# Kernel tuning notes

Hardware: AMD Instinct MI355X
Metric: run time of the kernel (lower is better)

## Reference

```python
import jax, jax.numpy as jnp
import numpy as np

TOP_K = 2


def setup_inputs() -> dict:
    key = jax.random.key(0)
    k1, k2, k3, k4 = jax.random.split(key, 4)
    B, S, D, F, E = 4, 512, 512, 2048, 16
    hidden_states = jax.random.normal(k1, (B, S, D), dtype=jnp.float32)
    gate_weight = jax.random.normal(k2, (E, D), dtype=jnp.float32) * 0.02
    w1 = jax.random.normal(k3, (E, F, D), dtype=jnp.float32) * 0.02
    w2 = jax.random.normal(k4, (E, D, F), dtype=jnp.float32) * 0.02
    return {"hidden_states": hidden_states, "gate_weight": gate_weight, "w1": w1, "w2": w2}


def reference(hidden_states, gate_weight, w1, w2):
    B, S, D = hidden_states.shape
    E = gate_weight.shape[0]
    x = hidden_states.reshape(-1, D)  # [T, D]

    # fused_top_k_routing: logits = x @ Wg^T, top-k, softmax over the k values
    gate_logits = x @ gate_weight.T  # [T, E]
    top_vals, top_idx = jax.lax.top_k(gate_logits, TOP_K)  # [T, k]
    routing_w = jax.nn.softmax(top_vals, axis=-1)  # [T, k]

    # _prepare_expert_inputs: token t goes to expert e iff e in its top-k
    mask = jnp.any(top_idx[:, :, None] == jnp.arange(E)[None, None, :], axis=1)  # [T, E] bool

    # Expert FFN on routed tokens, computed densely over (token, expert) pairs then masked.
    # h[t,e,f] = silu(x_t @ W1_e^T)
    h = jax.nn.silu(jnp.einsum('td,efd->tef', x, w1))  # [T, E, F]
    counts = jnp.sum(mask, axis=0)  # [E]
    h_sum = jnp.einsum('tef,te->ef', h, mask.astype(h.dtype))  # [E, F]
    h_mean = h_sum / jnp.maximum(counts, 1)[:, None].astype(h.dtype)

    # fused_expert_scatter_gather uses expert_outputs[e].mean(dim=0);
    # mean(W2 @ act) = W2 @ mean(act) since W2 is linear.
    y_mean = jnp.einsum('ef,edf->ed', h_mean, w2)  # [E, D]
    y_mean = jnp.where((counts > 0)[:, None], y_mean, 0.0)

    # per-token combine: sum_k w_k * mean_output[expert_k]
    out = jnp.einsum('tk,tkd->td', routing_w, y_mean[top_idx])  # [T, D]
    return out.reshape(B, S, D)
```

## Files before the change

kernel.cpp:

```cpp
#include <hip/hip_runtime.h>

#define NTOK   2048
#define DIM    512
#define FDIM   2048
#define NEXP   16
#define CAP    768
#define BT2    128
#define NTB    (CAP / BT2)

typedef __bf16 bf16x8 __attribute__((ext_vector_type(8)));
typedef float  floatx4 __attribute__((ext_vector_type(4)));

#define WS_COUNTS    0
#define WS_TOPIDX    4096
#define WS_ROUTW     20480
#define WS_HMEAN     36864
#define WS_YMEAN     167936
#define WS_XG        200704
#define WS_ZERO_BYTES 167936


__device__ __forceinline__ void async_lds16(const void* g, void* l) {
    __builtin_amdgcn_global_load_lds(
        (const __attribute__((address_space(1))) void*)g,
        (__attribute__((address_space(3))) void*)l, 16, 0, 0);
}

__global__ __launch_bounds__(256) void k1_route_gather(
    const float* __restrict__ x, const float* __restrict__ gw,
    int* __restrict__ counts, int* __restrict__ top_idx,
    float* __restrict__ routw, __bf16* __restrict__ Xg)
{
    __shared__ float xt[16 * DIM];
    __shared__ float lg[16][17];
    __shared__ int   gde[16][2];
    __shared__ int   gdp[16][2];
    const int tid = threadIdx.x;
    const int t0  = blockIdx.x * 16;

    {
        const float4* src = (const float4*)(x + (size_t)t0 * DIM);
        float4* dst = (float4*)xt;
        #pragma unroll
        for (int i = 0; i < 8; ++i) dst[i * 256 + tid] = src[i * 256 + tid];
    }
    __syncthreads();

    {
        const int tl = tid >> 4, e = tid & 15;
        const float4* xr = (const float4*)(xt + tl * DIM);
        const float4* gr = (const float4*)(gw + e * DIM);
        float acc = 0.f;
        #pragma unroll 8
        for (int j = 0; j < DIM / 4; ++j) {
            float4 a = xr[j], b = gr[j];
            acc += a.x * b.x + a.y * b.y + a.z * b.z + a.w * b.w;
        }
        lg[tl][e] = acc;
    }
    __syncthreads();

    if (tid < 16) {
        const int tl = tid;
        float v0 = -1e30f, v1 = -1e30f; int i0 = 0, i1 = 0;
        #pragma unroll
        for (int e = 0; e < NEXP; ++e) {
            float v = lg[tl][e];
            if (v > v0)      { v1 = v0; i1 = i0; v0 = v; i0 = e; }
            else if (v > v1) { v1 = v;  i1 = e; }
        }
        float e1 = __expf(v1 - v0);
        float w0 = 1.f / (1.f + e1);
        float w1 = 1.f - w0;
        const int t = t0 + tl;
        top_idx[t * 2]     = i0; top_idx[t * 2 + 1] = i1;
        routw[t * 2]       = w0; routw[t * 2 + 1]   = w1;
        int p0 = atomicAdd(counts + i0, 1);
        int p1 = atomicAdd(counts + i1, 1);
        gde[tl][0] = (p0 < CAP) ? i0 : -1;  gdp[tl][0] = p0;
        gde[tl][1] = (p1 < CAP) ? i1 : -1;  gdp[tl][1] = p1;
    }
    __syncthreads();

    #pragma unroll
    for (int it = 0; it < 8; ++it) {
        int j   = it * 256 + tid;
        int row = j >> 6, s = j & 63;
        int tl  = row >> 1, k = row & 1;
        int e   = gde[tl][k];
        if (e >= 0) {
            int p = gdp[tl][k];
            const float* srcf = xt + tl * DIM + s * 8;
            float4 a = *(const float4*)srcf;
            float4 b = *(const float4*)(srcf + 4);
            bf16x8 v;
            v[0] = (__bf16)a.x; v[1] = (__bf16)a.y; v[2] = (__bf16)a.z; v[3] = (__bf16)a.w;
            v[4] = (__bf16)b.x; v[5] = (__bf16)b.y; v[6] = (__bf16)b.z; v[7] = (__bf16)b.w;
            *(bf16x8*)(Xg + ((size_t)(e * 64 + s) * CAP + p) * 8) = v;
        }
    }
}

__global__ __launch_bounds__(256) void k2_expert_ffn(
    const float* __restrict__ w1, const __bf16* __restrict__ Xg,
    const int* __restrict__ counts, float* __restrict__ hmean)
{
    __shared__ __align__(16) __bf16 w1s[2][8 * 65 * 8];
    __shared__ __align__(16) __bf16 xs[2][8 * 128 * 8];
    __shared__ float hred[64][2];

    const int tid = threadIdx.x;
    const int bid = blockIdx.x;
    const int tb  = bid >> 9;
    const int rem9 = bid & 511;
    const int e   = rem9 & 15;
    const int f0  = (rem9 >> 4) * 64;
    const int cnt = min(counts[e], CAP);
    if (tb * BT2 >= cnt) return;
    const bool tail = (tb * BT2 + BT2 > cnt);
    const int rem  = cnt - tb * BT2;
    const float inv = 1.f / (float)cnt;

    const int wv   = tid >> 6;
    const int lane = tid & 63;
    const int q    = lane >> 4;
    const int l15  = lane & 15;
    const int fsub = (wv & 1) * 32;
    const int tsub = (wv >> 1) * 64;
    const int wvbase = tid & 192;

    floatx4 acc[2][4];
    #pragma unroll
    for (int a = 0; a < 2; ++a)
        #pragma unroll
        for (int b = 0; b < 4; ++b) acc[a][b] = (floatx4)0.f;

    auto stage = [&](int cc, int nb) {
        const int d0 = cc * 64;
        #pragma unroll
        for (int it = 0; it < 2; ++it) {
            int s = it * 256 + tid;
            int f = s >> 3, g8 = s & 7;
            const float* src = w1 + ((size_t)(e * FDIM + f0 + f)) * DIM + d0 + g8 * 8;
            float4 a = ((const float4*)src)[0];
            float4 b = ((const float4*)src)[1];
            bf16x8 v;
            v[0] = (__bf16)a.x; v[1] = (__bf16)a.y; v[2] = (__bf16)a.z; v[3] = (__bf16)a.w;
            v[4] = (__bf16)b.x; v[5] = (__bf16)b.y; v[6] = (__bf16)b.z; v[7] = (__bf16)b.w;
            *(bf16x8*)(&w1s[nb][((size_t)g8 * 65 + f) * 8]) = v;
        }
        if (!tail) {
            #pragma unroll
            for (int j = 0; j < 4; ++j) {
                int s = j * 256 + tid;
                int kg = s >> 7, tl = s & 127;
                const __bf16* g = Xg + (((size_t)(e * 64 + cc * 8 + kg)) * CAP + tb * BT2 + tl) * 8;
                __bf16* l = &xs[nb][(size_t)(j * 256 + wvbase) * 8];
                async_lds16(g, l);
            }
        } else {
            #pragma unroll
            for (int j = 0; j < 4; ++j) {
                int s = j * 256 + tid;
                int kg = s >> 7, tl = s & 127;
                uint4 v = make_uint4(0u, 0u, 0u, 0u);
                if (tl < rem)
                    v = *(const uint4*)(Xg + (((size_t)(e * 64 + cc * 8 + kg)) * CAP + tb * BT2 + tl) * 8);
                *(uint4*)(&xs[nb][(size_t)s * 8]) = v;
            }
        }
    };

    stage(0, 0);
    __syncthreads();

    int cur = 0;
    for (int c = 0; c < 8; ++c) {
        if (c < 7) stage(c + 1, cur ^ 1);
        const __bf16* w1c = w1s[cur];
        const __bf16* xc  = xs[cur];
        #pragma unroll
        for (int ks = 0; ks < 2; ++ks) {
            const int kg = ks * 4 + q;
            bf16x8 af0 = *(const bf16x8*)(w1c + ((size_t)kg * 65 + fsub + l15) * 8);
            bf16x8 af1 = *(const bf16x8*)(w1c + ((size_t)kg * 65 + fsub + 16 + l15) * 8);
            #pragma unroll
            for (int tt = 0; tt < 4; ++tt) {
                bf16x8 bfr = *(const bf16x8*)(xc + ((size_t)kg * 128 + tsub + tt * 16 + l15) * 8);
                acc[0][tt] = __builtin_amdgcn_mfma_f32_16x16x32_bf16(af0, bfr, acc[0][tt], 0, 0, 0);
                acc[1][tt] = __builtin_amdgcn_mfma_f32_16x16x32_bf16(af1, bfr, acc[1][tt], 0, 0, 0);
            }
        }
        __syncthreads();
        cur ^= 1;
    }

    float hs[8];
    #pragma unroll
    for (int i = 0; i < 8; ++i) hs[i] = 0.f;
    #pragma unroll
    for (int fa = 0; fa < 2; ++fa)
        #pragma unroll
        for (int tt = 0; tt < 4; ++tt)
            #pragma unroll
            for (int r = 0; r < 4; ++r) {
                float v = acc[fa][tt][r];
                hs[fa * 4 + r] += v / (1.f + __expf(-v));
            }

    #pragma unroll
    for (int i = 0; i < 8; ++i) {
        float v = hs[i];
        v += __shfl_xor(v, 1);
        v += __shfl_xor(v, 2);
        v += __shfl_xor(v, 4);
        v += __shfl_xor(v, 8);
        hs[i] = v;
    }
    if (l15 == 0) {
        #pragma unroll
        for (int fa = 0; fa < 2; ++fa)
            #pragma unroll
            for (int r = 0; r < 4; ++r) {
                int row = fsub + fa * 16 + q * 4 + r;
                hred[row][wv >> 1] = hs[fa * 4 + r];
            }
    }
    __syncthreads();
    if (tid < 64)
        atomicAdd(hmean + (size_t)e * FDIM + f0 + tid,
                  (hred[tid][0] + hred[tid][1]) * inv);
}

__global__ __launch_bounds__(256) void k3_ymean(
    const float* __restrict__ w2, const float* __restrict__ hmean,
    const int* __restrict__ counts, float* __restrict__ ymean)
{
    __shared__ float hl[FDIM];
    const int tid = threadIdx.x;
    const int bid = blockIdx.x;
    const int e   = bid >> 7;
    const int d0  = (bid & 127) * 4;

    {
        const float4* hg = (const float4*)(hmean + (size_t)e * FDIM);
        float4* hl4 = (float4*)hl;
        hl4[tid]       = hg[tid];
        hl4[256 + tid] = hg[256 + tid];
    }
    __syncthreads();

    const int wv = tid >> 6, lane = tid & 63;
    const int d = d0 + wv;
    const float4* wr  = (const float4*)(w2 + ((size_t)e * DIM + d) * FDIM);
    const float4* hl4 = (const float4*)hl;
    float acc = 0.f;
    #pragma unroll
    for (int i = 0; i < 8; ++i) {
        float4 a = wr[i * 64 + lane];
        float4 h = hl4[i * 64 + lane];
        acc += a.x * h.x + a.y * h.y + a.z * h.z + a.w * h.w;
    }
    #pragma unroll
    for (int m = 1; m < 64; m <<= 1) acc += __shfl_xor(acc, m);
    if (lane == 0)
        ymean[e * DIM + d] = (counts[e] > 0) ? acc : 0.f;
}

__global__ __launch_bounds__(256) void k4_combine(
    const int* __restrict__ top_idx, const float* __restrict__ routw,
    const float* __restrict__ ymean, float* __restrict__ out)
{
    const int idx = blockIdx.x * 256 + threadIdx.x;
    const int t = idx >> 7;
    const int c = idx & 127;
    const int i0 = top_idx[t * 2], i1 = top_idx[t * 2 + 1];
    const float w0 = routw[t * 2], w1 = routw[t * 2 + 1];
    float4 a = ((const float4*)(ymean + (size_t)i0 * DIM))[c];
    float4 b = ((const float4*)(ymean + (size_t)i1 * DIM))[c];
    float4 o;
    o.x = w0 * a.x + w1 * b.x;
    o.y = w0 * a.y + w1 * b.y;
    o.z = w0 * a.z + w1 * b.z;
    o.w = w0 * a.w + w1 * b.w;
    ((float4*)out)[idx] = o;
}

extern "C" void kernel_launch(void* const* d_in, const int* in_sizes, int n_in,
                              void* d_out, int out_size, void* d_ws, size_t ws_size,
                              hipStream_t stream)
{
    (void)in_sizes; (void)n_in; (void)out_size; (void)ws_size;
    const float* x  = (const float*)d_in[0];
    const float* gw = (const float*)d_in[1];
    const float* w1 = (const float*)d_in[2];
    const float* w2 = (const float*)d_in[3];
    float* out = (float*)d_out;

    char* ws = (char*)d_ws;
    int*    counts  = (int*)   (ws + WS_COUNTS);
    int*    top_idx = (int*)   (ws + WS_TOPIDX);
    float*  routw   = (float*) (ws + WS_ROUTW);
    float*  hmean   = (float*) (ws + WS_HMEAN);
    float*  ymean   = (float*) (ws + WS_YMEAN);
    __bf16* Xg      = (__bf16*)(ws + WS_XG);

    hipMemsetAsync(d_ws, 0, WS_ZERO_BYTES, stream);

    k1_route_gather<<<dim3(NTOK / 16), dim3(256), 0, stream>>>(x, gw, counts, top_idx, routw, Xg);
    k2_expert_ffn  <<<dim3(NTB * 32 * NEXP), dim3(256), 0, stream>>>(w1, Xg, counts, hmean);
    k3_ymean       <<<dim3(NEXP * 128), dim3(256), 0, stream>>>(w2, hmean, counts, ymean);
    k4_combine     <<<dim3(NTOK * DIM / 4 / 256), dim3(256), 0, stream>>>(top_idx, routw, ymean, out);
}
```

Measured before the change: 216.5 us.

## Replace LDS-staged double buffering in expert FFN with direct global fragment loads

The expert FFN kernel no longer stages W1 and gathered X tiles through double-buffered shared memory. Each wave now loads its MFMA fragments straight from global memory, converting W1 fp32 to bf16 in registers, and runs a fully unrolled 16-step K loop with no barriers. To make out-of-range token reads safe, the zeroed workspace region is widened to cover the whole gathered-X buffer, which adds memset traffic. The routing dot product also gets two independent accumulators. The trade-off is removing LDS traffic and syncs at the cost of redundant global or L2 loads shared across waves and less coalesced access.

```diff
diff --git a/kernel.cpp b/kernel.cpp
--- a/kernel.cpp
+++ b/kernel.cpp
@@ -17,14 +17,9 @@
 #define WS_HMEAN     36864
 #define WS_YMEAN     167936
 #define WS_XG        200704
-#define WS_ZERO_BYTES 167936
-
-
-__device__ __forceinline__ void async_lds16(const void* g, void* l) {
-    __builtin_amdgcn_global_load_lds(
-        (const __attribute__((address_space(1))) void*)g,
-        (__attribute__((address_space(3))) void*)l, 16, 0, 0);
-}
+#define WS_XG_BYTES  (NEXP * 64 * CAP * 16)
+#define WS_ZERO_BYTES (WS_XG + WS_XG_BYTES)
+
 
 __global__ __launch_bounds__(256) void k1_route_gather(
     const float* __restrict__ x, const float* __restrict__ gw,
@@ -50,13 +45,15 @@
         const int tl = tid >> 4, e = tid & 15;
         const float4* xr = (const float4*)(xt + tl * DIM);
         const float4* gr = (const float4*)(gw + e * DIM);
-        float acc = 0.f;
+        float acc0 = 0.f, acc1 = 0.f;
         #pragma unroll 8
-        for (int j = 0; j < DIM / 4; ++j) {
-            float4 a = xr[j], b = gr[j];
-            acc += a.x * b.x + a.y * b.y + a.z * b.z + a.w * b.w;
-        }
-        lg[tl][e] = acc;
+        for (int j = 0; j < DIM / 4; j += 2) {
+            float4 a = xr[j],     b = gr[j];
+            float4 c = xr[j + 1], d = gr[j + 1];
+            acc0 += a.x * b.x + a.y * b.y + a.z * b.z + a.w * b.w;
+            acc1 += c.x * d.x + c.y * d.y + c.z * d.z + c.w * d.w;
+        }
+        lg[tl][e] = acc0 + acc1;
     }
     __syncthreads();
 
@@ -105,8 +102,6 @@
     const float* __restrict__ w1, const __bf16* __restrict__ Xg,
     const int* __restrict__ counts, float* __restrict__ hmean)
 {
-    __shared__ __align__(16) __bf16 w1s[2][8 * 65 * 8];
-    __shared__ __align__(16) __bf16 xs[2][8 * 128 * 8];
     __shared__ float hred[64][2];
 
     const int tid = threadIdx.x;
@@ -117,8 +112,6 @@
     const int f0  = (rem9 >> 4) * 64;
     const int cnt = min(counts[e], CAP);
     if (tb * BT2 >= cnt) return;
-    const bool tail = (tb * BT2 + BT2 > cnt);
-    const int rem  = cnt - tb * BT2;
     const float inv = 1.f / (float)cnt;
 
     const int wv   = tid >> 6;
@@ -127,7 +120,10 @@
     const int l15  = lane & 15;
     const int fsub = (wv & 1) * 32;
     const int tsub = (wv >> 1) * 64;
-    const int wvbase = tid & 192;
+
+    const float* a0p = w1 + ((size_t)(e * FDIM + f0 + fsub + l15)) * DIM + q * 8;
+    const float* a1p = a0p + 16 * DIM;
+    const __bf16* bp0 = Xg + ((size_t)(e * 64 + q) * CAP + tb * BT2 + tsub + l15) * 8;
 
     floatx4 acc[2][4];
     #pragma unroll
@@ -135,64 +131,26 @@
         #pragma unroll
         for (int b = 0; b < 4; ++b) acc[a][b] = (floatx4)0.f;
 
-    auto stage = [&](int cc, int nb) {
-        const int d0 = cc * 64;
-        #pragma unroll
-        for (int it = 0; it < 2; ++it) {
-            int s = it * 256 + tid;
-            int f = s >> 3, g8 = s & 7;
-            const float* src = w1 + ((size_t)(e * FDIM + f0 + f)) * DIM + d0 + g8 * 8;
-            float4 a = ((const float4*)src)[0];
-            float4 b = ((const float4*)src)[1];
-            bf16x8 v;
-            v[0] = (__bf16)a.x; v[1] = (__bf16)a.y; v[2] = (__bf16)a.z; v[3] = (__bf16)a.w;
-            v[4] = (__bf16)b.x; v[5] = (__bf16)b.y; v[6] = (__bf16)b.z; v[7] = (__bf16)b.w;
-            *(bf16x8*)(&w1s[nb][((size_t)g8 * 65 + f) * 8]) = v;
-        }
-        if (!tail) {
-            #pragma unroll
-            for (int j = 0; j < 4; ++j) {
-                int s = j * 256 + tid;
-                int kg = s >> 7, tl = s & 127;
-                const __bf16* g = Xg + (((size_t)(e * 64 + cc * 8 + kg)) * CAP + tb * BT2 + tl) * 8;
-                __bf16* l = &xs[nb][(size_t)(j * 256 + wvbase) * 8];
-                async_lds16(g, l);
-            }
-        } else {
-            #pragma unroll
-            for (int j = 0; j < 4; ++j) {
-                int s = j * 256 + tid;
-                int kg = s >> 7, tl = s & 127;
-                uint4 v = make_uint4(0u, 0u, 0u, 0u);
-                if (tl < rem)
-                    v = *(const uint4*)(Xg + (((size_t)(e * 64 + cc * 8 + kg)) * CAP + tb * BT2 + tl) * 8);
-                *(uint4*)(&xs[nb][(size_t)s * 8]) = v;
-            }
-        }
-    };
-
-    stage(0, 0);
-    __syncthreads();
-
-    int cur = 0;
-    for (int c = 0; c < 8; ++c) {
-        if (c < 7) stage(c + 1, cur ^ 1);
-        const __bf16* w1c = w1s[cur];
-        const __bf16* xc  = xs[cur];
-        #pragma unroll
-        for (int ks = 0; ks < 2; ++ks) {
-            const int kg = ks * 4 + q;
-            bf16x8 af0 = *(const bf16x8*)(w1c + ((size_t)kg * 65 + fsub + l15) * 8);
-            bf16x8 af1 = *(const bf16x8*)(w1c + ((size_t)kg * 65 + fsub + 16 + l15) * 8);
-            #pragma unroll
-            for (int tt = 0; tt < 4; ++tt) {
-                bf16x8 bfr = *(const bf16x8*)(xc + ((size_t)kg * 128 + tsub + tt * 16 + l15) * 8);
-                acc[0][tt] = __builtin_amdgcn_mfma_f32_16x16x32_bf16(af0, bfr, acc[0][tt], 0, 0, 0);
-                acc[1][tt] = __builtin_amdgcn_mfma_f32_16x16x32_bf16(af1, bfr, acc[1][tt], 0, 0, 0);
-            }
-        }
-        __syncthreads();
-        cur ^= 1;
+    #pragma unroll
+    for (int kg = 0; kg < 16; ++kg) {
+        const int k0 = kg * 32;
+        float4 a0a = *(const float4*)(a0p + k0);
+        float4 a0b = *(const float4*)(a0p + k0 + 4);
+        float4 a1a = *(const float4*)(a1p + k0);
+        float4 a1b = *(const float4*)(a1p + k0 + 4);
+        bf16x8 af0, af1;
+        af0[0] = (__bf16)a0a.x; af0[1] = (__bf16)a0a.y; af0[2] = (__bf16)a0a.z; af0[3] = (__bf16)a0a.w;
+        af0[4] = (__bf16)a0b.x; af0[5] = (__bf16)a0b.y; af0[6] = (__bf16)a0b.z; af0[7] = (__bf16)a0b.w;
+        af1[0] = (__bf16)a1a.x; af1[1] = (__bf16)a1a.y; af1[2] = (__bf16)a1a.z; af1[3] = (__bf16)a1a.w;
+        af1[4] = (__bf16)a1b.x; af1[5] = (__bf16)a1b.y; af1[6] = (__bf16)a1b.z; af1[7] = (__bf16)a1b.w;
+
+        const __bf16* bp = bp0 + (size_t)kg * 4 * CAP * 8;
+        #pragma unroll
+        for (int tt = 0; tt < 4; ++tt) {
+            bf16x8 bv = *(const bf16x8*)(bp + tt * 16 * 8);
+            acc[0][tt] = __builtin_amdgcn_mfma_f32_16x16x32_bf16(af0, bv, acc[0][tt], 0, 0, 0);
+            acc[1][tt] = __builtin_amdgcn_mfma_f32_16x16x32_bf16(af1, bv, acc[1][tt], 0, 0, 0);
+        }
     }
 
     float hs[8];
```

Measured after the change: 243.7 us. 1.13x slower.
